# Kernel optimization log

Hardware: AMD Instinct MI355X
Metric: run time of the kernel (lower is better)

The kernel has to match this reference:

```python
import jax, jax.numpy as jnp
import numpy as np

N_NODES = 100000
D = 128
R = 4          # number of edge types
E = 500000     # edges per relation


def setup_inputs() -> dict:
    key = jax.random.key(0)
    ks = jax.random.split(key, 6)
    x = jax.random.normal(ks[0], (N_NODES, D), dtype=jnp.float32)
    src = jax.random.randint(ks[1], (R, E), 0, N_NODES)
    dst = jax.random.randint(ks[2], (R, E), 0, N_NODES)
    # Per-relation SAGEConv (mean) parameters: fc_self, fc_neigh, bias
    scale = 1.0 / np.sqrt(D)
    Wself = jax.random.normal(ks[3], (R, D, D), dtype=jnp.float32) * scale
    Wneigh = jax.random.normal(ks[4], (R, D, D), dtype=jnp.float32) * scale
    b = jnp.zeros((R, D), dtype=jnp.float32)
    return {"x": x, "src": src, "dst": dst, "Wself": Wself, "Wneigh": Wneigh, "b": b}


def reference(x, src, dst, Wself, Wneigh, b):
    """HetGraphLayer with SAGE(mean) convs per relation + mean channel combine.

    x:     [N, D] node features (same node set for all relations)
    src:   [R, E] int source node ids per relation
    dst:   [R, E] int destination node ids per relation
    Wself, Wneigh: [R, D, D]; b: [R, D]
    """
    N = x.shape[0]

    def one_relation(s, d, Ws, Wn, bb):
        msg = x[s]                                                   # [E, D] gather
        summed = jax.ops.segment_sum(msg, d, num_segments=N)         # [N, D] scatter-add
        cnt = jax.ops.segment_sum(jnp.ones(s.shape, x.dtype), d, num_segments=N)
        neigh = summed / jnp.maximum(cnt, 1.0)[:, None]              # mean aggregation
        return x @ Ws + neigh @ Wn + bb                              # SAGEConv(mean)

    rel_embs = jax.vmap(one_relation)(src, dst, Wself, Wneigh, b)    # [R, N, D]
    # ChannelCombine('mean'): average across relation channels
    return rel_embs.mean(axis=0)                                     # [N, D]
```

## Files before the change

kernel.cpp:

```cpp
#include <hip/hip_runtime.h>
#include <hip/hip_bf16.h>
#include <stdint.h>

#define N_NODES 100000
#define DIM 128
#define NREL 4
#define NEDGE 500000
#define M_FLAT (NREL * N_NODES)
#define TOT_E (NREL * NEDGE)
#define BSLOT 1024
#define NBK ((M_FLAT + BSLOT - 1) / BSLOT)
#define CAP 8192
#define CHUNK 8192
#define NBSC ((TOT_E + CHUNK - 1) / CHUNK)
#define NQ (N_NODES * DIM / 4)
#define XB_BATCH 8
#define NBXB ((NQ + 256 * XB_BATCH - 1) / (256 * XB_BATCH))
#define NBPREP ((5 * DIM * DIM + 255) / 256)

typedef __attribute__((ext_vector_type(8))) short short8;
typedef __attribute__((ext_vector_type(4))) float f32x4;
typedef __attribute__((ext_vector_type(2))) float f32x2;

__device__ __forceinline__ unsigned short f2bf(float f) {
  unsigned int u = __float_as_uint(f);
  u += 0x7fffu + ((u >> 16) & 1u);
  return (unsigned short)(u >> 16);
}

__global__ __launch_bounds__(256) void pre_kernel(
    const int* __restrict__ src, const int* __restrict__ dst,
    int* __restrict__ bcnt, unsigned int* __restrict__ gpairs,
    const float* __restrict__ x, unsigned short* __restrict__ xb,
    const float* __restrict__ Ws, const float* __restrict__ Wn,
    const float* __restrict__ bv, unsigned short* __restrict__ Wt,
    float* __restrict__ biasc) {
  __shared__ unsigned int buf[CHUNK];
  __shared__ unsigned short barr[CHUNK];
  __shared__ int hist[NBK];
  __shared__ int sbase[NBK];
  __shared__ int lcur[NBK];
  __shared__ int gbase[NBK];
  __shared__ int part[256];
  int bid = blockIdx.x;
  int tid = threadIdx.x;

  if (bid < NBSC) {
    int base = bid * CHUNK;
    int m = TOT_E - base; if (m > CHUNK) m = CHUNK;
    for (int i = tid; i < NBK; i += 256) { hist[i] = 0; lcur[i] = 0; }
    __syncthreads();
    unsigned int pk[CHUNK / 256];
    int bk[CHUNK / 256];
#pragma unroll
    for (int k = 0; k < CHUNK / 256; ++k) {
      int i = k * 256 + tid;
      int idx = base + i;
      int b = -1; unsigned int p = 0;
      if (i < m) {
        int r = idx / NEDGE;
        int fl = r * N_NODES + dst[idx];
        b = fl >> 10;
        p = ((unsigned int)(fl & (BSLOT - 1)) << 17) | (unsigned int)src[idx];
        atomicAdd(&hist[b], 1);
      }
      pk[k] = p; bk[k] = b;
    }
    __syncthreads();
    {
      int vA = hist[tid];
      part[tid] = vA;
      __syncthreads();
      for (int o = 1; o < 256; o <<= 1) {
        int u = (tid >= o) ? part[tid - o] : 0;
        __syncthreads();
        part[tid] += u;
        __syncthreads();
      }
      sbase[tid] = part[tid] - vA;
      int totalA = part[255];
      __syncthreads();
      int vB = (256 + tid < NBK) ? hist[256 + tid] : 0;
      part[tid] = vB;
      __syncthreads();
      for (int o = 1; o < 256; o <<= 1) {
        int u = (tid >= o) ? part[tid - o] : 0;
        __syncthreads();
        part[tid] += u;
        __syncthreads();
      }
      if (256 + tid < NBK) sbase[256 + tid] = totalA + part[tid] - vB;
    }
    __syncthreads();
#pragma unroll
    for (int k = 0; k < CHUNK / 256; ++k) {
      if (bk[k] >= 0) {
        int pos = sbase[bk[k]] + atomicAdd(&lcur[bk[k]], 1);
        buf[pos] = pk[k];
        barr[pos] = (unsigned short)bk[k];
      }
    }
    __syncthreads();
    for (int i = tid; i < NBK; i += 256)
      if (hist[i] > 0) gbase[i] = i * CAP + atomicAdd(&bcnt[i], hist[i]) - sbase[i];
    __syncthreads();
    for (int j = tid; j < m; j += 256)
      gpairs[gbase[barr[j]] + j] = buf[j];
  } else if (bid < NBSC + NBXB) {
    int base = (bid - NBSC) * (256 * XB_BATCH);
    float4 v[XB_BATCH];
#pragma unroll
    for (int k = 0; k < XB_BATCH; ++k) {
      int i = base + k * 256 + tid;
      if (i < NQ) v[k] = ((const float4*)x)[i];
    }
#pragma unroll
    for (int k = 0; k < XB_BATCH; ++k) {
      int i = base + k * 256 + tid;
      if (i < NQ) {
        ushort4 s;
        s.x = f2bf(v[k].x); s.y = f2bf(v[k].y); s.z = f2bf(v[k].z); s.w = f2bf(v[k].w);
        ((ushort4*)xb)[i] = s;
      }
    }
  } else {
    int t3 = (bid - NBSC - NBXB) * 256 + tid;
    if (t3 < 5 * DIM * DIM) {
      int b = t3 / (DIM * DIM);
      int idx = t3 - b * DIM * DIM;
      int k = idx >> 7, n = idx & 127;
      float v;
      if (b == 0)
        v = 0.25f * (Ws[idx] + Ws[DIM * DIM + idx] + Ws[2 * DIM * DIM + idx] + Ws[3 * DIM * DIM + idx]);
      else
        v = 0.25f * Wn[(b - 1) * DIM * DIM + idx];
      int ks = k >> 5, kq = (k >> 3) & 3, j = k & 7;
      int ct = n >> 4, lr = n & 15;
      int lane = kq * 16 + lr;
      Wt[((((b * 4 + ks) * 8) + ct) * 64 + lane) * 8 + j] = f2bf(v);
    }
    if (t3 < DIM)
      biasc[t3] = 0.25f * (bv[t3] + bv[DIM + t3] + bv[2 * DIM + t3] + bv[3 * DIM + t3]);
  }
}

__global__ __launch_bounds__(256) void bfill_kernel(
    const unsigned int* __restrict__ gpairs, const int* __restrict__ bcnt,
    int* __restrict__ offs, int* __restrict__ ssrc) {
  __shared__ int lcnt[BSLOT];
  __shared__ int lofs[BSLOT];
  __shared__ int lcur[BSLOT];
  __shared__ int part[256];
  __shared__ int sbuf[CAP];
  int b = blockIdx.x;
  int tid = threadIdx.x;
  int base = b * CAP;
  int cntb = bcnt[b];
  int flBase = b << 10;
  int flCount = M_FLAT - flBase; if (flCount > BSLOT) flCount = BSLOT;
  for (int i = tid; i < BSLOT; i += 256) { lcnt[i] = 0; lcur[i] = 0; }
  __syncthreads();
  for (int j = tid; j < cntb; j += 256)
    atomicAdd(&lcnt[gpairs[base + j] >> 17], 1);
  __syncthreads();
  int vals[4]; int s0 = 0;
#pragma unroll
  for (int k = 0; k < 4; ++k) { vals[k] = lcnt[tid * 4 + k]; s0 += vals[k]; }
  part[tid] = s0;
  __syncthreads();
  for (int o = 1; o < 256; o <<= 1) {
    int u = (tid >= o) ? part[tid - o] : 0;
    __syncthreads();
    part[tid] += u;
    __syncthreads();
  }
  int excl = part[tid] - s0;
#pragma unroll
  for (int k = 0; k < 4; ++k) { lofs[tid * 4 + k] = excl; excl += vals[k]; }
  __syncthreads();
  for (int i = tid; i <= flCount; i += 256)
    offs[b * (BSLOT + 1) + i] = base + ((i < BSLOT) ? lofs[i] : cntb);
  for (int j = tid; j < cntb; j += 256) {
    unsigned int p = gpairs[base + j];
    int li = p >> 17;
    int pos = atomicAdd(&lcur[li], 1);
    sbuf[lofs[li] + pos] = (int)(p & 0x1FFFFu);
  }
  __syncthreads();
  for (int j = tid; j < cntb; j += 256)
    ssrc[base + j] = sbuf[j];
}

__global__ __launch_bounds__(256) void aggregate_kernel(
    const unsigned int* __restrict__ xb32, const int* __restrict__ ssrc,
    const int* __restrict__ offs, unsigned int* __restrict__ agg32) {
  int lane = threadIdx.x & 63;
  int n = blockIdx.x * 4 + (int)__builtin_amdgcn_readfirstlane(threadIdx.x >> 6);
  if (n >= N_NODES) return;

  int start[NREL], end[NREL];
#pragma unroll
  for (int r = 0; r < NREL; ++r) {
    int fl = r * N_NODES + n;
    int oidx = fl + (fl >> 10);
    start[r] = __builtin_amdgcn_readfirstlane(offs[oidx]);
    end[r] = __builtin_amdgcn_readfirstlane(offs[oidx + 1]);
  }

  unsigned int v[NREL][8];
#pragma unroll
  for (int r = 0; r < NREL; ++r) {
    int s = start[r], m = end[r] - s;
#pragma unroll
    for (int k = 0; k < 8; ++k) {
      int ea = (m > 0) ? (s + ((k < m) ? k : (m - 1))) : 0;
      int idx = ssrc[ea];
      v[r][k] = xb32[((unsigned)idx << 6) | (unsigned)lane];
    }
  }

  f32x2 acc[NREL];
#pragma unroll
  for (int r = 0; r < NREL; ++r) {
    f32x2 a = {0.f, 0.f};
    int m = end[r] - start[r];
#pragma unroll
    for (int k = 0; k < 8; ++k) {
      unsigned int u = (k < m) ? v[r][k] : 0u;
      f32x2 d;
      d.x = __uint_as_float(u << 16);
      d.y = __uint_as_float(u & 0xffff0000u);
      a += d;
    }
    acc[r] = a;
  }

  bool anyTail = ((end[0] - start[0]) > 8) | ((end[1] - start[1]) > 8) |
                 ((end[2] - start[2]) > 8) | ((end[3] - start[3]) > 8);
  if (anyTail) {
#pragma unroll
    for (int r = 0; r < NREL; ++r) {
      for (int e = start[r] + 8; e < end[r]; e += 8) {
        int m = end[r] - e;
        unsigned int w[8];
#pragma unroll
        for (int k = 0; k < 8; ++k) {
          int idx = ssrc[e + ((k < m) ? k : 0)];
          w[k] = xb32[((unsigned)idx << 6) | (unsigned)lane];
        }
#pragma unroll
        for (int k = 0; k < 8; ++k) {
          unsigned int u = (k < m) ? w[k] : 0u;
          f32x2 d;
          d.x = __uint_as_float(u << 16);
          d.y = __uint_as_float(u & 0xffff0000u);
          acc[r] += d;
        }
      }
    }
  }

#pragma unroll
  for (int r = 0; r < NREL; ++r) {
    int c = end[r] - start[r];
    float inv = __builtin_amdgcn_rcpf((float)(c > 0 ? c : 1));
    float lo = acc[r].x * inv, hi = acc[r].y * inv;
    unsigned int packed;
    asm("v_cvt_pk_bf16_f32 %0, %1, %2" : "=v"(packed) : "v"(lo), "v"(hi));
    agg32[((size_t)r * N_NODES + n) * 64 + lane] = packed;
  }
}

__global__ __launch_bounds__(256) void gemm_kernel(
    const unsigned short* __restrict__ xb, const unsigned short* __restrict__ Wt,
    const float* __restrict__ biasc, float* __restrict__ out,
    const unsigned short* __restrict__ agg) {
  __shared__ short8 Bs[2048];
  int tid = threadIdx.x;
  int lane = tid & 63;
  int wv = __builtin_amdgcn_readfirstlane(tid >> 6);
  int bandRow = blockIdx.x * 128 + wv * 32;
  int valid = bandRow < N_NODES;
  int ldRow = valid ? bandRow : 0;
  int quad = lane >> 4;
  int lr = lane & 15;
  const short8* Bp = (const short8*)Wt;

  float bias8[8];
#pragma unroll
  for (int ct = 0; ct < 8; ++ct) bias8[ct] = biasc[ct * 16 + lr];

  f32x4 zero = {0.f, 0.f, 0.f, 0.f};
  f32x4 acc[2][8];
#pragma unroll
  for (int rt = 0; rt < 2; ++rt)
#pragma unroll
    for (int ct = 0; ct < 8; ++ct) acc[rt][ct] = zero;

#pragma unroll
  for (int p = 0; p < 8; ++p) Bs[p * 256 + tid] = Bp[p * 256 + tid];
  short8 a0c[4], a1c[4];
  {
    const unsigned short* rowp = xb + (size_t)(ldRow + lr) * DIM;
#pragma unroll
    for (int ks = 0; ks < 4; ++ks) {
      int k0 = ks * 32 + quad * 8;
      a0c[ks] = *(const short8*)(rowp + k0);
      a1c[ks] = *(const short8*)(rowp + 16 * DIM + k0);
    }
  }
  __syncthreads();

#pragma unroll
  for (int bi = 0; bi < 5; ++bi) {
    short8 a0n[4], a1n[4];
    if (bi < 4) {
      const unsigned short* rowp = agg + (size_t)bi * N_NODES * DIM + (size_t)(ldRow + lr) * DIM;
#pragma unroll
      for (int ks = 0; ks < 4; ++ks) {
        int k0 = ks * 32 + quad * 8;
        a0n[ks] = *(const short8*)(rowp + k0);
        a1n[ks] = *(const short8*)(rowp + 16 * DIM + k0);
      }
    }
#pragma unroll
    for (int ks = 0; ks < 4; ++ks) {
#pragma unroll
      for (int ct = 0; ct < 8; ++ct) {
        short8 bf = Bs[(ks * 8 + ct) * 64 + lane];
        acc[0][ct] = __builtin_amdgcn_mfma_f32_16x16x32_bf16(a0c[ks], bf, acc[0][ct], 0, 0, 0);
        acc[1][ct] = __builtin_amdgcn_mfma_f32_16x16x32_bf16(a1c[ks], bf, acc[1][ct], 0, 0, 0);
      }
    }
    if (bi < 4) {
      __syncthreads();
#pragma unroll
      for (int p = 0; p < 8; ++p)
        Bs[p * 256 + tid] = Bp[(size_t)(bi + 1) * 2048 + p * 256 + tid];
      __syncthreads();
#pragma unroll
      for (int ks = 0; ks < 4; ++ks) { a0c[ks] = a0n[ks]; a1c[ks] = a1n[ks]; }
    }
  }

  if (valid) {
#pragma unroll
    for (int rt = 0; rt < 2; ++rt)
#pragma unroll
      for (int i = 0; i < 4; ++i) {
        int g = bandRow + rt * 16 + quad * 4 + i;
#pragma unroll
        for (int ct = 0; ct < 8; ++ct)
          out[(size_t)g * DIM + ct * 16 + lr] = acc[rt][ct][i] + bias8[ct];
      }
  }
}

extern "C" void kernel_launch(void* const* d_in, const int* in_sizes, int n_in,
                              void* d_out, int out_size, void* d_ws, size_t ws_size,
                              hipStream_t stream) {
  const float* x = (const float*)d_in[0];
  const int* src = (const int*)d_in[1];
  const int* dst = (const int*)d_in[2];
  const float* Wself = (const float*)d_in[3];
  const float* Wneigh = (const float*)d_in[4];
  const float* bv = (const float*)d_in[5];
  float* out = (float*)d_out;

  char* ws = (char*)d_ws;
  size_t off = 0;
  int* bcnt = (int*)(ws + off);        off += 2048;
  unsigned short* Wt = (unsigned short*)(ws + off);  off += 5 * DIM * DIM * 2;
  float* biasc = (float*)(ws + off);   off += DIM * 4;
  int* offs = (int*)(ws + off);        off += ((size_t)NBK * (BSLOT + 1) * 4 + 15) & ~15;
  unsigned short* xb = (unsigned short*)(ws + off);  off += (size_t)N_NODES * DIM * 2;
  unsigned int* gpairs = (unsigned int*)(ws + off);  off += (size_t)NBK * CAP * 4;
  int* ssrc = (int*)(ws + off);        off += (size_t)NBK * CAP * 4;
  unsigned short* agg = (unsigned short*)(ws + off);

  hipMemsetAsync(bcnt, 0, 2048, stream);
  pre_kernel<<<NBSC + NBXB + NBPREP, 256, 0, stream>>>(src, dst, bcnt, gpairs,
                                                       x, xb, Wself, Wneigh, bv, Wt, biasc);
  bfill_kernel<<<NBK, 256, 0, stream>>>(gpairs, bcnt, offs, ssrc);
  aggregate_kernel<<<(N_NODES + 3) / 4, 256, 0, stream>>>((const unsigned int*)xb, ssrc,
                                                          offs, (unsigned int*)agg);
  gemm_kernel<<<(N_NODES + 127) / 128, 256, 0, stream>>>(xb, Wt, biasc, out, agg);
}
```

Measured before the change: 291.9 us.

## Split aggregation into per-relation launches and use nontemporal loads/stores

The aggregate kernel now handles one relation per launch, with four launches in sequence, instead of processing all four relations in one wave with 32 gathers in flight. It uses a simple loop of 8-edge batches, which removes the fixed 8-load prefetch per relation. Nontemporal hints are added to the agg stores, the GEMM activation loads and the output stores to reduce cache pollution. This lowers register use and wasted gathers for low-degree nodes, but gives up memory-level parallelism across relations and adds launch overhead.

```diff
diff --git a/kernel.cpp b/kernel.cpp
--- a/kernel.cpp
+++ b/kernel.cpp
@@ -193,82 +193,40 @@
 
 __global__ __launch_bounds__(256) void aggregate_kernel(
     const unsigned int* __restrict__ xb32, const int* __restrict__ ssrc,
-    const int* __restrict__ offs, unsigned int* __restrict__ agg32) {
+    const int* __restrict__ offs, unsigned int* __restrict__ agg32, int r) {
   int lane = threadIdx.x & 63;
   int n = blockIdx.x * 4 + (int)__builtin_amdgcn_readfirstlane(threadIdx.x >> 6);
   if (n >= N_NODES) return;
 
-  int start[NREL], end[NREL];
-#pragma unroll
-  for (int r = 0; r < NREL; ++r) {
-    int fl = r * N_NODES + n;
-    int oidx = fl + (fl >> 10);
-    start[r] = __builtin_amdgcn_readfirstlane(offs[oidx]);
-    end[r] = __builtin_amdgcn_readfirstlane(offs[oidx + 1]);
-  }
-
-  unsigned int v[NREL][8];
-#pragma unroll
-  for (int r = 0; r < NREL; ++r) {
-    int s = start[r], m = end[r] - s;
+  int fl = r * N_NODES + n;
+  int oidx = fl + (fl >> 10);
+  int start = __builtin_amdgcn_readfirstlane(offs[oidx]);
+  int end = __builtin_amdgcn_readfirstlane(offs[oidx + 1]);
+  int c = end - start;
+
+  f32x2 acc = {0.f, 0.f};
+  for (int e = start; e < end; e += 8) {
+    int m = end - e;
+    unsigned int v[8];
 #pragma unroll
     for (int k = 0; k < 8; ++k) {
-      int ea = (m > 0) ? (s + ((k < m) ? k : (m - 1))) : 0;
-      int idx = ssrc[ea];
-      v[r][k] = xb32[((unsigned)idx << 6) | (unsigned)lane];
-    }
-  }
-
-  f32x2 acc[NREL];
-#pragma unroll
-  for (int r = 0; r < NREL; ++r) {
-    f32x2 a = {0.f, 0.f};
-    int m = end[r] - start[r];
+      int idx = ssrc[e + ((k < m) ? k : 0)];
+      v[k] = xb32[((unsigned)idx << 6) | (unsigned)lane];
+    }
 #pragma unroll
     for (int k = 0; k < 8; ++k) {
-      unsigned int u = (k < m) ? v[r][k] : 0u;
+      unsigned int u = (k < m) ? v[k] : 0u;
       f32x2 d;
       d.x = __uint_as_float(u << 16);
       d.y = __uint_as_float(u & 0xffff0000u);
-      a += d;
-    }
-    acc[r] = a;
-  }
-
-  bool anyTail = ((end[0] - start[0]) > 8) | ((end[1] - start[1]) > 8) |
-                 ((end[2] - start[2]) > 8) | ((end[3] - start[3]) > 8);
-  if (anyTail) {
-#pragma unroll
-    for (int r = 0; r < NREL; ++r) {
-      for (int e = start[r] + 8; e < end[r]; e += 8) {
-        int m = end[r] - e;
-        unsigned int w[8];
-#pragma unroll
-        for (int k = 0; k < 8; ++k) {
-          int idx = ssrc[e + ((k < m) ? k : 0)];
-          w[k] = xb32[((unsigned)idx << 6) | (unsigned)lane];
-        }
-#pragma unroll
-        for (int k = 0; k < 8; ++k) {
-          unsigned int u = (k < m) ? w[k] : 0u;
-          f32x2 d;
-          d.x = __uint_as_float(u << 16);
-          d.y = __uint_as_float(u & 0xffff0000u);
-          acc[r] += d;
-        }
-      }
-    }
-  }
-
-#pragma unroll
-  for (int r = 0; r < NREL; ++r) {
-    int c = end[r] - start[r];
-    float inv = __builtin_amdgcn_rcpf((float)(c > 0 ? c : 1));
-    float lo = acc[r].x * inv, hi = acc[r].y * inv;
-    unsigned int packed;
-    asm("v_cvt_pk_bf16_f32 %0, %1, %2" : "=v"(packed) : "v"(lo), "v"(hi));
-    agg32[((size_t)r * N_NODES + n) * 64 + lane] = packed;
-  }
+      acc += d;
+    }
+  }
+  float inv = __builtin_amdgcn_rcpf((float)(c > 0 ? c : 1));
+  float lo = acc.x * inv, hi = acc.y * inv;
+  unsigned int packed;
+  asm("v_cvt_pk_bf16_f32 %0, %1, %2" : "=v"(packed) : "v"(lo), "v"(hi));
+  __builtin_nontemporal_store(packed, &agg32[((size_t)r * N_NODES + n) * 64 + lane]);
 }
 
 __global__ __launch_bounds__(256) void gemm_kernel(
@@ -305,8 +263,8 @@
 #pragma unroll
     for (int ks = 0; ks < 4; ++ks) {
       int k0 = ks * 32 + quad * 8;
-      a0c[ks] = *(const short8*)(rowp + k0);
-      a1c[ks] = *(const short8*)(rowp + 16 * DIM + k0);
+      a0c[ks] = __builtin_nontemporal_load((const short8*)(rowp + k0));
+      a1c[ks] = __builtin_nontemporal_load((const short8*)(rowp + 16 * DIM + k0));
     }
   }
   __syncthreads();
@@ -319,8 +277,8 @@
 #pragma unroll
       for (int ks = 0; ks < 4; ++ks) {
         int k0 = ks * 32 + quad * 8;
-        a0n[ks] = *(const short8*)(rowp + k0);
-        a1n[ks] = *(const short8*)(rowp + 16 * DIM + k0);
+        a0n[ks] = __builtin_nontemporal_load((const short8*)(rowp + k0));
+        a1n[ks] = __builtin_nontemporal_load((const short8*)(rowp + 16 * DIM + k0));
       }
     }
 #pragma unroll
@@ -351,7 +309,8 @@
         int g = bandRow + rt * 16 + quad * 4 + i;
 #pragma unroll
         for (int ct = 0; ct < 8; ++ct)
-          out[(size_t)g * DIM + ct * 16 + lr] = acc[rt][ct][i] + bias8[ct];
+          __builtin_nontemporal_store(acc[rt][ct][i] + bias8[ct],
+                                      &out[(size_t)g * DIM + ct * 16 + lr]);
       }
   }
 }
@@ -382,7 +341,10 @@
   pre_kernel<<<NBSC + NBXB + NBPREP, 256, 0, stream>>>(src, dst, bcnt, gpairs,
                                                        x, xb, Wself, Wneigh, bv, Wt, biasc);
   bfill_kernel<<<NBK, 256, 0, stream>>>(gpairs, bcnt, offs, ssrc);
-  aggregate_kernel<<<(N_NODES + 3) / 4, 256, 0, stream>>>((const unsigned int*)xb, ssrc,
-                                                          offs, (unsigned int*)agg);
+
+  int gAgg = (N_NODES + 3) / 4;
+  for (int r = 0; r < NREL; ++r)
+    aggregate_kernel<<<gAgg, 256, 0, stream>>>((const unsigned int*)xb, ssrc, offs,
+                                               (unsigned int*)agg, r);
   gemm_kernel<<<(N_NODES + 127) / 128, 256, 0, stream>>>(xb, Wt, biasc, out, agg);
 }
```

Result: slower. 312.6 us (+7.1%).
